# Performance work log

Hardware: AMD Instinct MI355X
Metric: run time of the kernel (lower is better)

The kernel has to match this reference:

```python
import jax, jax.numpy as jnp
import numpy as np

D_MODEL = 1024
NUM_HEADS = 16
D_K = D_MODEL // NUM_HEADS  # 64
MAX_SEQ_LEN = 2048
THETA = 10000.0
BATCH = 2
SEQ = 2048


def _rope_tables():
    # freqs: [d_k/2], positions: [max_seq_len] -> angles [max_seq_len, d_k/2]
    freqs = THETA ** (-jnp.arange(0, D_K, 2, dtype=jnp.float32) / D_K)
    positions = jnp.arange(MAX_SEQ_LEN, dtype=jnp.float32)[:, None]
    angles = positions * freqs[None, :]
    return jnp.cos(angles), jnp.sin(angles)


def _apply_rope(x, token_positions, cos_cached, sin_cached):
    # x: [..., seq, d_k]; token_positions: [seq]
    cos = cos_cached[token_positions]  # [seq, d_k/2]
    sin = sin_cached[token_positions]
    x_even = x[..., ::2]
    x_odd = x[..., 1::2]
    r_even = x_even * cos - x_odd * sin
    r_odd = x_even * sin + x_odd * cos
    # interleave even/odd back into last dim
    out = jnp.stack([r_even, r_odd], axis=-1)
    return out.reshape(x.shape)


def setup_inputs() -> dict:
    key = jax.random.key(0)
    ks = jax.random.split(key, 5)
    scale = 1.0 / np.sqrt(D_MODEL)
    in_features = jax.random.normal(ks[0], (BATCH, SEQ, D_MODEL), dtype=jnp.float32)
    q_proj = jax.random.normal(ks[1], (D_MODEL, D_MODEL), dtype=jnp.float32) * scale
    k_proj = jax.random.normal(ks[2], (D_MODEL, D_MODEL), dtype=jnp.float32) * scale
    v_proj = jax.random.normal(ks[3], (D_MODEL, D_MODEL), dtype=jnp.float32) * scale
    o_proj = jax.random.normal(ks[4], (D_MODEL, D_MODEL), dtype=jnp.float32) * scale
    mask = jnp.tril(jnp.ones((SEQ, SEQ), dtype=bool))  # causal
    token_positions = jnp.arange(SEQ, dtype=jnp.int32)
    return {
        "in_features": in_features,
        "q_proj": q_proj,
        "k_proj": k_proj,
        "v_proj": v_proj,
        "o_proj": o_proj,
        "mask": mask,
        "token_positions": token_positions,
    }


def reference(in_features, q_proj, k_proj, v_proj, o_proj, mask, token_positions):
    B, S, _ = in_features.shape
    cos_cached, sin_cached = _rope_tables()
    # fused QKV projection (same math as x @ cat(Wq,Wk,Wv).T then chunk)
    q = jnp.einsum("bsd,ed->bse", in_features, q_proj)
    k = jnp.einsum("bsd,ed->bse", in_features, k_proj)
    v = jnp.einsum("bsd,ed->bse", in_features, v_proj)
    # ... seq (h d) -> ... h seq d
    q = q.reshape(B, S, NUM_HEADS, D_K).transpose(0, 2, 1, 3)
    k = k.reshape(B, S, NUM_HEADS, D_K).transpose(0, 2, 1, 3)
    v = v.reshape(B, S, NUM_HEADS, D_K).transpose(0, 2, 1, 3)
    q = _apply_rope(q, token_positions, cos_cached, sin_cached)
    k = _apply_rope(k, token_positions, cos_cached, sin_cached)
    scores = jnp.einsum("bhqd,bhkd->bhqk", q, k) / np.sqrt(D_K)
    scores = jnp.where(mask, scores, -jnp.inf)
    attn = jax.nn.softmax(scores, axis=-1)
    out = jnp.einsum("bhqk,bhkd->bhqd", attn, v)
    # ... h seq d -> ... seq (h d)
    concat = out.transpose(0, 2, 1, 3).reshape(B, S, D_MODEL)
    return jnp.einsum("bsd,ed->bse", concat, o_proj)
```

## Files before the change

### kernel.cpp

```cpp
#include <hip/hip_runtime.h>
#include <cstdint>

#define D_MODEL 1024
#define NHEADS 16
#define DKH 64
#define SEQL 2048
#define NBATCH 2
#define NROWS (NBATCH * SEQL)

typedef __bf16 bf16;
typedef __bf16 bf16x2 __attribute__((ext_vector_type(2)));
typedef __bf16 bf16x4 __attribute__((ext_vector_type(4)));
typedef __bf16 bf16x8 __attribute__((ext_vector_type(8)));
typedef float f32x4 __attribute__((ext_vector_type(4)));

static __device__ __forceinline__ f32x4 mfma16(bf16x8 a, bf16x8 b, f32x4 c) {
  return __builtin_amdgcn_mfma_f32_16x16x32_bf16(a, b, c, 0, 0, 0);
}

static __device__ __forceinline__ void gload_lds16(const bf16* g, bf16* l) {
  __builtin_amdgcn_global_load_lds(
      (const __attribute__((address_space(1))) void*)g,
      (__attribute__((address_space(3))) void*)l, 16, 0, 0);
}

static __device__ __forceinline__ unsigned pack_bf16(float a, float b) {
  unsigned au = __builtin_bit_cast(unsigned, a) + 0x8000u;
  unsigned bu = __builtin_bit_cast(unsigned, b) + 0x8000u;
  return __builtin_amdgcn_perm(bu, au, 0x07060302u);
}

__global__ __launch_bounds__(256) void convert_kernel(
    const float* __restrict__ x, const float* __restrict__ wq,
    const float* __restrict__ wk, const float* __restrict__ wv,
    const float* __restrict__ wo, bf16* __restrict__ xb,
    bf16* __restrict__ wqb, bf16* __restrict__ wkb, bf16* __restrict__ wvb,
    bf16* __restrict__ wob) {
  int i4 = blockIdx.x * 256 + threadIdx.x;
  const float* src;
  bf16* dst;
  int off;
  if (i4 < (NROWS * D_MODEL / 4)) {
    src = x; dst = xb; off = i4;
  } else {
    int j = i4 - NROWS * D_MODEL / 4;
    int sel = j >> 18;
    off = j & ((1 << 18) - 1);
    src = sel == 0 ? wq : sel == 1 ? wk : sel == 2 ? wv : wo;
    dst = sel == 0 ? wqb : sel == 1 ? wkb : sel == 2 ? wvb : wob;
  }
  float4 v = ((const float4*)src)[off];
  bf16x4 o;
  o[0] = (bf16)v.x; o[1] = (bf16)v.y; o[2] = (bf16)v.z; o[3] = (bf16)v.w;
  ((bf16x4*)dst)[off] = o;
}

template <int BM, int BN, typename OutT>
__device__ __forceinline__ void gemm_body64(const bf16* __restrict__ A,
                                            const bf16* __restrict__ Bm,
                                            OutT* __restrict__ C, int M, int N,
                                            int K) {
  constexpr int MT = BM / 32, NT = BN / 32;
  constexpr int CA = BM / 32, CB = BN / 32;
  __shared__ bf16 As[BM * 64];
  __shared__ bf16 Bs[BN * 64];
  const int t = threadIdx.x;
  const int wave = t >> 6, lane = t & 63;
  const int quad = lane >> 4, l16 = lane & 15;
  const int wm = (wave >> 1) * (MT * 16), wn = (wave & 1) * (NT * 16);
  const int bm = blockIdx.x * BM, bn = blockIdx.y * BN;

  f32x4 acc[MT][NT];
  for (int i = 0; i < MT; i++)
    for (int j = 0; j < NT; j++)
      for (int r = 0; r < 4; r++) acc[i][j][r] = 0.0f;

  for (int k0 = 0; k0 < K; k0 += 64) {
    for (int j = 0; j < CA; j++) {
      int s = (wave * CA + j) * 64 + lane;
      int srow = s >> 3, scol = (s & 7) ^ (srow & 7);
      gload_lds16(&A[(size_t)(bm + srow) * K + k0 + scol * 8],
                  &As[(wave * CA + j) * 512]);
    }
    for (int j = 0; j < CB; j++) {
      int s = (wave * CB + j) * 64 + lane;
      int srow = s >> 3, scol = (s & 7) ^ (srow & 7);
      gload_lds16(&Bm[(size_t)(bn + srow) * K + k0 + scol * 8],
                  &Bs[(wave * CB + j) * 512]);
    }
    __syncthreads();
    for (int kh = 0; kh < 2; kh++) {
      const int kc = kh * 4 + quad;
      bf16x8 af[MT], bfr[NT];
      for (int mt = 0; mt < MT; mt++) {
        int row = wm + mt * 16 + l16;
        af[mt] = *(bf16x8*)&As[row * 64 + (kc ^ (row & 7)) * 8];
      }
      for (int nt = 0; nt < NT; nt++) {
        int row = wn + nt * 16 + l16;
        bfr[nt] = *(bf16x8*)&Bs[row * 64 + (kc ^ (row & 7)) * 8];
      }
      for (int mt = 0; mt < MT; mt++)
        for (int nt = 0; nt < NT; nt++)
          acc[mt][nt] = mfma16(af[mt], bfr[nt], acc[mt][nt]);
    }
    __syncthreads();
  }
  for (int mt = 0; mt < MT; mt++)
    for (int nt = 0; nt < NT; nt++)
      for (int r = 0; r < 4; r++) {
        int row = bm + wm + mt * 16 + quad * 4 + r;
        int col = bn + wn + nt * 16 + l16;
        C[(size_t)row * N + col] = (OutT)acc[mt][nt][r];
      }
}

__global__ __launch_bounds__(256, 3) void qkv_gemm(
    const bf16* __restrict__ A, const bf16* __restrict__ B0,
    const bf16* __restrict__ B1, const bf16* __restrict__ B2,
    bf16* __restrict__ C0, bf16* __restrict__ C1, bf16* __restrict__ C2) {
  const bf16* Bm = blockIdx.z == 0 ? B0 : blockIdx.z == 1 ? B1 : B2;
  bf16* C = blockIdx.z == 0 ? C0 : blockIdx.z == 1 ? C1 : C2;
  gemm_body64<128, 128, bf16>(A, Bm, C, NROWS, D_MODEL, D_MODEL);
}

__global__ __launch_bounds__(256, 3) void o_gemm(const bf16* __restrict__ A,
                                                 const bf16* __restrict__ Bm,
                                                 float* __restrict__ C) {
  gemm_body64<64, 128, float>(A, Bm, C, NROWS, D_MODEL, D_MODEL);
}

__global__ __launch_bounds__(256) void rope_kernel(bf16* __restrict__ Q,
                                                   bf16* __restrict__ Kb,
                                                   const int* __restrict__ tpos) {
  const int NG = NROWS * (D_MODEL / 8);
  int idx = blockIdx.x * 256 + threadIdx.x;
  bf16* buf = Q;
  int i = idx;
  float qsc = 0.125f * 1.44269504f;
  if (idx >= NG) { buf = Kb; i = idx - NG; qsc = 1.0f; }
  int row = i >> 7;
  int g = i & 127;
  int p0 = (g & 7) * 4;
  int col = (g >> 3) * DKH + p0 * 2;
  int s = row & (SEQL - 1);
  float pos = (float)tpos[s];
  size_t o = (size_t)row * D_MODEL + col;
  bf16x8 v = *(bf16x8*)&buf[o];
  bf16x8 out;
  for (int j = 0; j < 4; j++) {
    float freq = exp2f((float)(p0 + j) * (-13.28771238f / 32.0f));
    float ang = pos * freq;
    float sn, cs;
    __sincosf(ang, &sn, &cs);
    cs *= qsc; sn *= qsc;
    float e = (float)v[2 * j], od = (float)v[2 * j + 1];
    out[2 * j]     = (bf16)(e * cs - od * sn);
    out[2 * j + 1] = (bf16)(e * sn + od * cs);
  }
  *(bf16x8*)&buf[o] = out;
}

__global__ __launch_bounds__(256) void attn_kernel(
    const bf16* __restrict__ Q, const bf16* __restrict__ K,
    const bf16* __restrict__ V, float* __restrict__ O0,
    float* __restrict__ O1, float* __restrict__ O2, float* __restrict__ O3,
    float* __restrict__ L0, float* __restrict__ L1, float* __restrict__ L2,
    float* __restrict__ L3) {
  const int t = threadIdx.x;
  const int wave = t >> 6, lane = t & 63;
  const int quad = lane >> 4, l16 = lane & 15;

  const int id = blockIdx.x;
  const int bh = id & 31;
  const int c = 39 - (id >> 5);
  int qt, piece, np;
  if (c < 4)       { qt = c;                 piece = 0;            np = 1; }
  else if (c < 12) { int e = c - 4;  qt = 4 + (e >> 1); piece = e & 1; np = 2; }
  else if (c < 24) { int e = c - 12; qt = 8 + e / 3;    piece = e % 3; np = 3; }
  else             { int e = c - 24; qt = 12 + (e >> 2); piece = e & 3; np = 4; }
  const int total = qt + 1, bas = total / np, rem = total % np;
  const int len = bas + (piece < rem ? 1 : 0);
  const int k0 = piece * bas + (piece < rem ? piece : rem);
  const int k1 = k0 + len - 1;

  const int b = bh >> 4, h = bh & 15;
  const int q_base = qt * 128;
  const size_t base = (size_t)b * SEQL * D_MODEL + h * DKH;

  __shared__ bf16 Ks[128 * 72];
  __shared__ bf16 Vt[64 * 136];
  __shared__ bf16 Pw[4 * 32 * 68];

  for (int i = 0; i < 4; i++) {
    int idx = t + i * 256;
    int row = idx >> 3, c8 = (idx & 7) * 8;
    *(bf16x8*)&Ks[row * 72 + c8] =
        *(const bf16x8*)&Q[base + (size_t)(q_base + row) * D_MODEL + c8];
  }
  __syncthreads();
  bf16x8 qb[2][2];
  for (int n = 0; n < 2; n++) {
    int row = wave * 32 + n * 16 + l16;
    qb[n][0] = *(bf16x8*)&Ks[row * 72 + quad * 8];
    qb[n][1] = *(bf16x8*)&Ks[row * 72 + 32 + quad * 8];
  }
  __syncthreads();

  bf16x8 ones;
  for (int j = 0; j < 8; j++) ones[j] = (bf16)1.0f;

  f32x4 oaccT[2][4];
  f32x4 lacc[2];
  for (int n = 0; n < 2; n++) {
    for (int r = 0; r < 4; r++) lacc[n][r] = 0.0f;
    for (int dt = 0; dt < 4; dt++)
      for (int r = 0; r < 4; r++) oaccT[n][dt][r] = 0.0f;
  }

  const int kp = t & 63;
  const int dgbase = t >> 6;
  bf16* P = &Pw[wave * 32 * 68];

  for (int kv = k0; kv <= k1; kv++) {
    const int kv_base = kv * 128;
    for (int i = 0; i < 4; i++) {
      int idx = t + i * 256;
      int row = idx >> 3, c8 = (idx & 7) * 8;
      *(bf16x8*)&Ks[row * 72 + c8] =
          *(const bf16x8*)&K[base + (size_t)(kv_base + row) * D_MODEL + c8];
    }
    for (int i = 0; i < 2; i++) {
      int d0 = (dgbase + 4 * i) * 8;
      const bf16* vsrc = &V[base + (size_t)(kv_base + 2 * kp) * D_MODEL + d0];
      bf16x8 g0 = *(const bf16x8*)vsrc;
      bf16x8 g1 = *(const bf16x8*)(vsrc + D_MODEL);
      for (int j = 0; j < 8; j++) {
        bf16x2 w2;
        w2[0] = g0[j];
        w2[1] = g1[j];
        *(bf16x2*)&Vt[(d0 + j) * 136 + 2 * kp] = w2;
      }
    }
    __syncthreads();

    const bool diag = (kv == qt);
    for (int h2 = 0; h2 < 2; h2++) {
      f32x4 sT[2][4];
      for (int n = 0; n < 2; n++)
        for (int mtl = 0; mtl < 4; mtl++)
          for (int r = 0; r < 4; r++) sT[n][mtl][r] = 0.0f;
      for (int mtl = 0; mtl < 4; mtl++) {
        int krow = h2 * 64 + mtl * 16 + l16;
        bf16x8 kf0 = *(bf16x8*)&Ks[krow * 72 + quad * 8];
        bf16x8 kf1 = *(bf16x8*)&Ks[krow * 72 + 32 + quad * 8];
        for (int n = 0; n < 2; n++) {
          sT[n][mtl] = mfma16(kf0, qb[n][0], sT[n][mtl]);
          sT[n][mtl] = mfma16(kf1, qb[n][1], sT[n][mtl]);
        }
      }
      if (diag) {
        for (int n = 0; n < 2; n++) {
          int q_loc = wave * 32 + n * 16 + l16;
          for (int mtl = 0; mtl < 4; mtl++) {
            int key0 = h2 * 64 + mtl * 16 + quad * 4;
            for (int r = 0; r < 4; r++)
              if (key0 + r > q_loc) sT[n][mtl][r] = -1e30f;
          }
        }
      }
      for (int n = 0; n < 2; n++)
        for (int mtl = 0; mtl < 4; mtl++) {
          float p0 = exp2f(sT[n][mtl][0]);
          float p1 = exp2f(sT[n][mtl][1]);
          float p2 = exp2f(sT[n][mtl][2]);
          float p3 = exp2f(sT[n][mtl][3]);
          uint2 u;
          u.x = pack_bf16(p0, p1);
          u.y = pack_bf16(p2, p3);
          *(uint2*)&P[(n * 16 + l16) * 68 + mtl * 16 + quad * 4] = u;
        }
      for (int c2 = 0; c2 < 2; c2++) {
        bf16x8 pf[2];
        for (int n = 0; n < 2; n++)
          pf[n] = *(bf16x8*)&P[(n * 16 + l16) * 68 + c2 * 32 + quad * 8];
        for (int n = 0; n < 2; n++) lacc[n] = mfma16(ones, pf[n], lacc[n]);
        for (int dt = 0; dt < 4; dt++) {
          bf16x8 vf = *(bf16x8*)&Vt[(dt * 16 + l16) * 136 + h2 * 64 +
                                    c2 * 32 + quad * 8];
          for (int n = 0; n < 2; n++)
            oaccT[n][dt] = mfma16(vf, pf[n], oaccT[n][dt]);
        }
      }
    }
    __syncthreads();
  }

  float* Ob;
  float* Lb;
  int rbase, roff;
  if (piece == 0)      { Ob = O0; Lb = L0; rbase = SEQL;        roff = 0; }
  else if (piece == 1) { Ob = O1; Lb = L1; rbase = SEQL - 512;  roff = 512; }
  else if (piece == 2) { Ob = O2; Lb = L2; rbase = SEQL - 1024; roff = 1024; }
  else                 { Ob = O3; Lb = L3; rbase = SEQL - 1536; roff = 1536; }
  for (int n = 0; n < 2; n++) {
    int qrow = q_base + wave * 32 + n * 16 + l16;
    size_t orow = (size_t)b * rbase + (qrow - roff);
    if (quad == 0) Lb[orow * NHEADS + h] = lacc[n][0];
    for (int dt = 0; dt < 4; dt++)
      *(f32x4*)&Ob[orow * D_MODEL + h * DKH + dt * 16 + quad * 4] =
          oaccT[n][dt];
  }
}

__global__ __launch_bounds__(256) void normalize_kernel(
    const float* __restrict__ O0, const float* __restrict__ O1,
    const float* __restrict__ O2, const float* __restrict__ O3,
    const float* __restrict__ L0, const float* __restrict__ L1,
    const float* __restrict__ L2, const float* __restrict__ L3,
    bf16* __restrict__ Cc) {
  int i4 = blockIdx.x * 256 + threadIdx.x;
  int row = i4 >> 8;
  int c0 = (i4 & 255) * 4;
  int s = row & (SEQL - 1);
  int b = row >> 11;
  int h = c0 >> 6;
  float l = L0[(size_t)row * NHEADS + h];
  f32x4 v = *(const f32x4*)&O0[(size_t)row * D_MODEL + c0];
  if (s >= 512) {
    size_t r1 = (size_t)b * (SEQL - 512) + (s - 512);
    l += L1[r1 * NHEADS + h];
    f32x4 u = *(const f32x4*)&O1[r1 * D_MODEL + c0];
    for (int r = 0; r < 4; r++) v[r] += u[r];
  }
  if (s >= 1024) {
    size_t r2 = (size_t)b * (SEQL - 1024) + (s - 1024);
    l += L2[r2 * NHEADS + h];
    f32x4 u = *(const f32x4*)&O2[r2 * D_MODEL + c0];
    for (int r = 0; r < 4; r++) v[r] += u[r];
  }
  if (s >= 1536) {
    size_t r3 = (size_t)b * (SEQL - 1536) + (s - 1536);
    l += L3[r3 * NHEADS + h];
    f32x4 u = *(const f32x4*)&O3[r3 * D_MODEL + c0];
    for (int r = 0; r < 4; r++) v[r] += u[r];
  }
  float inv = 1.0f / l;
  bf16x4 o;
  o[0] = (bf16)(v[0] * inv);
  o[1] = (bf16)(v[1] * inv);
  o[2] = (bf16)(v[2] * inv);
  o[3] = (bf16)(v[3] * inv);
  *(bf16x4*)&Cc[(size_t)row * D_MODEL + c0] = o;
}

extern "C" void kernel_launch(void* const* d_in, const int* in_sizes, int n_in,
                              void* d_out, int out_size, void* d_ws,
                              size_t ws_size, hipStream_t stream) {
  const float* x = (const float*)d_in[0];
  const float* wq = (const float*)d_in[1];
  const float* wk = (const float*)d_in[2];
  const float* wv = (const float*)d_in[3];
  const float* wo = (const float*)d_in[4];
  const int* tpos = (const int*)d_in[6];
  float* out = (float*)d_out;

  char* p = (char*)d_ws;
  bf16* xb  = (bf16*)p; p += (size_t)NROWS * D_MODEL * 2;
  bf16* wqb = (bf16*)p; p += (size_t)D_MODEL * D_MODEL * 2;
  bf16* wkb = (bf16*)p; p += (size_t)D_MODEL * D_MODEL * 2;
  bf16* wvb = (bf16*)p; p += (size_t)D_MODEL * D_MODEL * 2;
  bf16* wob = (bf16*)p; p += (size_t)D_MODEL * D_MODEL * 2;
  bf16* Qb  = (bf16*)p; p += (size_t)NROWS * D_MODEL * 2;
  bf16* Kb  = (bf16*)p; p += (size_t)NROWS * D_MODEL * 2;
  bf16* Vb  = (bf16*)p; p += (size_t)NROWS * D_MODEL * 2;
  bf16* Cc  = (bf16*)p; p += (size_t)NROWS * D_MODEL * 2;
  float* O0 = (float*)p; p += (size_t)NROWS * D_MODEL * 4;
  float* L0 = (float*)p; p += (size_t)NROWS * NHEADS * 4;
  float* O1 = (float*)p; p += (size_t)NBATCH * (SEQL - 512) * D_MODEL * 4;
  float* L1 = (float*)p; p += (size_t)NBATCH * (SEQL - 512) * NHEADS * 4;
  float* O2 = (float*)xb;
  float* O3 = (float*)wqb;
  float* L2 = (float*)wvb;
  float* L3 = (float*)wvb + (size_t)NBATCH * (SEQL - 1024) * NHEADS;

  convert_kernel<<<8192, 256, 0, stream>>>(x, wq, wk, wv, wo, xb, wqb, wkb,
                                           wvb, wob);
  qkv_gemm<<<dim3(NROWS / 128, D_MODEL / 128, 3), 256, 0, stream>>>(
      xb, wqb, wkb, wvb, Qb, Kb, Vb);
  rope_kernel<<<4096, 256, 0, stream>>>(Qb, Kb, tpos);
  attn_kernel<<<1280, 256, 0, stream>>>(Qb, Kb, Vb, O0, O1, O2, O3, L0, L1,
                                        L2, L3);
  normalize_kernel<<<NROWS * D_MODEL / 1024, 256, 0, stream>>>(
      O0, O1, O2, O3, L0, L1, L2, L3, Cc);
  o_gemm<<<dim3(NROWS / 64, D_MODEL / 128), 256, 0, stream>>>(Cc, wob, out);
}
```

Before: 224.8 us.

## Produce V transposed from QKV GEMM and stream K/V into LDS directly

The V projection is computed as Wv·Xᵀ by swapping GEMM operands, so V is stored transposed ([d_model, rows]) in global memory. The attention kernel then loads K, Q and the transposed V tiles with direct global-to-LDS loads into XOR-swizzled unpadded layouts. This replaces the per-iteration register transpose and scattered 2-element LDS stores of V. It also changes the GEMM body to take explicit tile origins and adjusts the P padding.

Result: faster. 203.5 us (-9.5%).

```diff
diff --git a/kernel.cpp b/kernel.cpp
--- a/kernel.cpp
+++ b/kernel.cpp
@@ -58,8 +58,8 @@
 template <int BM, int BN, typename OutT>
 __device__ __forceinline__ void gemm_body64(const bf16* __restrict__ A,
                                             const bf16* __restrict__ Bm,
-                                            OutT* __restrict__ C, int M, int N,
-                                            int K) {
+                                            OutT* __restrict__ C, int bm,
+                                            int bn, int N, int K) {
   constexpr int MT = BM / 32, NT = BN / 32;
   constexpr int CA = BM / 32, CB = BN / 32;
   __shared__ bf16 As[BM * 64];
@@ -68,7 +68,6 @@
   const int wave = t >> 6, lane = t & 63;
   const int quad = lane >> 4, l16 = lane & 15;
   const int wm = (wave >> 1) * (MT * 16), wn = (wave & 1) * (NT * 16);
-  const int bm = blockIdx.x * BM, bn = blockIdx.y * BN;
 
   f32x4 acc[MT][NT];
   for (int i = 0; i < MT; i++)
@@ -119,15 +118,22 @@
     const bf16* __restrict__ A, const bf16* __restrict__ B0,
     const bf16* __restrict__ B1, const bf16* __restrict__ B2,
     bf16* __restrict__ C0, bf16* __restrict__ C1, bf16* __restrict__ C2) {
-  const bf16* Bm = blockIdx.z == 0 ? B0 : blockIdx.z == 1 ? B1 : B2;
-  bf16* C = blockIdx.z == 0 ? C0 : blockIdx.z == 1 ? C1 : C2;
-  gemm_body64<128, 128, bf16>(A, Bm, C, NROWS, D_MODEL, D_MODEL);
+  if (blockIdx.z == 2) {
+    gemm_body64<128, 128, bf16>(B2, A, C2, blockIdx.y * 128, blockIdx.x * 128,
+                                NROWS, D_MODEL);
+  } else {
+    const bf16* Bm = blockIdx.z == 0 ? B0 : B1;
+    bf16* C = blockIdx.z == 0 ? C0 : C1;
+    gemm_body64<128, 128, bf16>(A, Bm, C, blockIdx.x * 128, blockIdx.y * 128,
+                                D_MODEL, D_MODEL);
+  }
 }
 
 __global__ __launch_bounds__(256, 3) void o_gemm(const bf16* __restrict__ A,
                                                  const bf16* __restrict__ Bm,
                                                  float* __restrict__ C) {
-  gemm_body64<64, 128, float>(A, Bm, C, NROWS, D_MODEL, D_MODEL);
+  gemm_body64<64, 128, float>(A, Bm, C, blockIdx.x * 64, blockIdx.y * 128,
+                              D_MODEL, D_MODEL);
 }
 
 __global__ __launch_bounds__(256) void rope_kernel(bf16* __restrict__ Q,
@@ -163,7 +169,7 @@
 
 __global__ __launch_bounds__(256) void attn_kernel(
     const bf16* __restrict__ Q, const bf16* __restrict__ K,
-    const bf16* __restrict__ V, float* __restrict__ O0,
+    const bf16* __restrict__ Vt_g, float* __restrict__ O0,
     float* __restrict__ O1, float* __restrict__ O2, float* __restrict__ O3,
     float* __restrict__ L0, float* __restrict__ L1, float* __restrict__ L2,
     float* __restrict__ L3) {
@@ -188,22 +194,25 @@
   const int q_base = qt * 128;
   const size_t base = (size_t)b * SEQL * D_MODEL + h * DKH;
 
-  __shared__ bf16 Ks[128 * 72];
-  __shared__ bf16 Vt[64 * 136];
-  __shared__ bf16 Pw[4 * 32 * 68];
+  __shared__ bf16 Ks[128 * 64];
+  __shared__ bf16 Vts[64 * 128];
+  __shared__ bf16 Pw[4 * 32 * 72];
+
+  const int r8 = lane >> 3, c8 = lane & 7;
+  const int r16 = lane >> 4, c16 = lane & 15;
 
   for (int i = 0; i < 4; i++) {
-    int idx = t + i * 256;
-    int row = idx >> 3, c8 = (idx & 7) * 8;
-    *(bf16x8*)&Ks[row * 72 + c8] =
-        *(const bf16x8*)&Q[base + (size_t)(q_base + row) * D_MODEL + c8];
+    int row = wave * 32 + i * 8 + r8;
+    int sc = c8 ^ (row & 7);
+    gload_lds16(&Q[base + (size_t)(q_base + row) * D_MODEL + sc * 8],
+                &Ks[(wave * 32 + i * 8) * 64]);
   }
   __syncthreads();
   bf16x8 qb[2][2];
   for (int n = 0; n < 2; n++) {
     int row = wave * 32 + n * 16 + l16;
-    qb[n][0] = *(bf16x8*)&Ks[row * 72 + quad * 8];
-    qb[n][1] = *(bf16x8*)&Ks[row * 72 + 32 + quad * 8];
+    qb[n][0] = *(bf16x8*)&Ks[row * 64 + (quad ^ (row & 7)) * 8];
+    qb[n][1] = *(bf16x8*)&Ks[row * 64 + ((4 + quad) ^ (row & 7)) * 8];
   }
   __syncthreads();
 
@@ -218,29 +227,22 @@
       for (int r = 0; r < 4; r++) oaccT[n][dt][r] = 0.0f;
   }
 
-  const int kp = t & 63;
-  const int dgbase = t >> 6;
-  bf16* P = &Pw[wave * 32 * 68];
+  bf16* P = &Pw[wave * 32 * 72];
+  const bf16* Vrow0 = &Vt_g[(size_t)(h * 64) * NROWS + b * SEQL];
 
   for (int kv = k0; kv <= k1; kv++) {
     const int kv_base = kv * 128;
     for (int i = 0; i < 4; i++) {
-      int idx = t + i * 256;
-      int row = idx >> 3, c8 = (idx & 7) * 8;
-      *(bf16x8*)&Ks[row * 72 + c8] =
-          *(const bf16x8*)&K[base + (size_t)(kv_base + row) * D_MODEL + c8];
-    }
-    for (int i = 0; i < 2; i++) {
-      int d0 = (dgbase + 4 * i) * 8;
-      const bf16* vsrc = &V[base + (size_t)(kv_base + 2 * kp) * D_MODEL + d0];
-      bf16x8 g0 = *(const bf16x8*)vsrc;
-      bf16x8 g1 = *(const bf16x8*)(vsrc + D_MODEL);
-      for (int j = 0; j < 8; j++) {
-        bf16x2 w2;
-        w2[0] = g0[j];
-        w2[1] = g1[j];
-        *(bf16x2*)&Vt[(d0 + j) * 136 + 2 * kp] = w2;
-      }
+      int row = wave * 32 + i * 8 + r8;
+      int sc = c8 ^ (row & 7);
+      gload_lds16(&K[base + (size_t)(kv_base + row) * D_MODEL + sc * 8],
+                  &Ks[(wave * 32 + i * 8) * 64]);
+    }
+    for (int i = 0; i < 4; i++) {
+      int d = wave * 16 + i * 4 + r16;
+      int sc = c16 ^ (d & 7);
+      gload_lds16(&Vrow0[(size_t)d * NROWS + kv_base + sc * 8],
+                  &Vts[(wave * 16 + i * 4) * 128]);
     }
     __syncthreads();
 
@@ -252,8 +254,8 @@
           for (int r = 0; r < 4; r++) sT[n][mtl][r] = 0.0f;
       for (int mtl = 0; mtl < 4; mtl++) {
         int krow = h2 * 64 + mtl * 16 + l16;
-        bf16x8 kf0 = *(bf16x8*)&Ks[krow * 72 + quad * 8];
-        bf16x8 kf1 = *(bf16x8*)&Ks[krow * 72 + 32 + quad * 8];
+        bf16x8 kf0 = *(bf16x8*)&Ks[krow * 64 + (quad ^ (krow & 7)) * 8];
+        bf16x8 kf1 = *(bf16x8*)&Ks[krow * 64 + ((4 + quad) ^ (krow & 7)) * 8];
         for (int n = 0; n < 2; n++) {
           sT[n][mtl] = mfma16(kf0, qb[n][0], sT[n][mtl]);
           sT[n][mtl] = mfma16(kf1, qb[n][1], sT[n][mtl]);
@@ -278,16 +280,17 @@
           uint2 u;
           u.x = pack_bf16(p0, p1);
           u.y = pack_bf16(p2, p3);
-          *(uint2*)&P[(n * 16 + l16) * 68 + mtl * 16 + quad * 4] = u;
+          *(uint2*)&P[(n * 16 + l16) * 72 + mtl * 16 + quad * 4] = u;
         }
       for (int c2 = 0; c2 < 2; c2++) {
         bf16x8 pf[2];
         for (int n = 0; n < 2; n++)
-          pf[n] = *(bf16x8*)&P[(n * 16 + l16) * 68 + c2 * 32 + quad * 8];
+          pf[n] = *(bf16x8*)&P[(n * 16 + l16) * 72 + c2 * 32 + quad * 8];
         for (int n = 0; n < 2; n++) lacc[n] = mfma16(ones, pf[n], lacc[n]);
+        const int kq = h2 * 8 + c2 * 4 + quad;
         for (int dt = 0; dt < 4; dt++) {
-          bf16x8 vf = *(bf16x8*)&Vt[(dt * 16 + l16) * 136 + h2 * 64 +
-                                    c2 * 32 + quad * 8];
+          int d = dt * 16 + l16;
+          bf16x8 vf = *(bf16x8*)&Vts[d * 128 + (kq ^ (d & 7)) * 8];
           for (int n = 0; n < 2; n++)
             oaccT[n][dt] = mfma16(vf, pf[n], oaccT[n][dt]);
         }
@@ -373,7 +376,7 @@
   bf16* wob = (bf16*)p; p += (size_t)D_MODEL * D_MODEL * 2;
   bf16* Qb  = (bf16*)p; p += (size_t)NROWS * D_MODEL * 2;
   bf16* Kb  = (bf16*)p; p += (size_t)NROWS * D_MODEL * 2;
-  bf16* Vb  = (bf16*)p; p += (size_t)NROWS * D_MODEL * 2;
+  bf16* Vt  = (bf16*)p; p += (size_t)NROWS * D_MODEL * 2;
   bf16* Cc  = (bf16*)p; p += (size_t)NROWS * D_MODEL * 2;
   float* O0 = (float*)p; p += (size_t)NROWS * D_MODEL * 4;
   float* L0 = (float*)p; p += (size_t)NROWS * NHEADS * 4;
@@ -387,9 +390,9 @@
   convert_kernel<<<8192, 256, 0, stream>>>(x, wq, wk, wv, wo, xb, wqb, wkb,
                                            wvb, wob);
   qkv_gemm<<<dim3(NROWS / 128, D_MODEL / 128, 3), 256, 0, stream>>>(
-      xb, wqb, wkb, wvb, Qb, Kb, Vb);
+      xb, wqb, wkb, wvb, Qb, Kb, Vt);
   rope_kernel<<<4096, 256, 0, stream>>>(Qb, Kb, tpos);
-  attn_kernel<<<1280, 256, 0, stream>>>(Qb, Kb, Vb, O0, O1, O2, O3, L0, L1,
+  attn_kernel<<<1280, 256, 0, stream>>>(Qb, Kb, Vt, O0, O1, O2, O3, L0, L1,
                                         L2, L3);
   normalize_kernel<<<NROWS * D_MODEL / 1024, 256, 0, stream>>>(
       O0, O1, O2, O3, L0, L1, L2, L3, Cc);
```
